# Kernel optimization log

Hardware: AMD Instinct MI355X
Metric: run time of the kernel (lower is better)

The kernel has to match this reference:

```python
import jax, jax.numpy as jnp
import numpy as np

DIM = 768
NUM_HEADS = 12
HEAD_DIM = DIM // NUM_HEADS
SCALE = HEAD_DIM ** -0.5
B, N = 8, 1024


def setup_inputs() -> dict:
    key = jax.random.key(0)
    k1, k2, k3, k4 = jax.random.split(key, 4)
    s = 1.0 / np.sqrt(DIM)
    return {
        "x": jax.random.normal(k1, (B, N, DIM), dtype=jnp.float32),
        "w_qkv": jax.random.normal(k2, (DIM, 3 * DIM), dtype=jnp.float32) * s,  # qkv_bias=False
        "w_proj": jax.random.normal(k3, (DIM, DIM), dtype=jnp.float32) * s,
        "b_proj": jax.random.normal(k4, (DIM,), dtype=jnp.float32) * 0.01,
    }


def reference(x, w_qkv, w_proj, b_proj):
    Bb, Nn, C = x.shape
    qkv = x @ w_qkv  # [B, N, 3C]
    qkv = qkv.reshape(Bb, Nn, 3, NUM_HEADS, HEAD_DIM)
    q = qkv[:, :, 0].transpose(0, 2, 1, 3)  # [B, H, N, d]
    k = qkv[:, :, 1].transpose(0, 2, 1, 3)
    v = qkv[:, :, 2].transpose(0, 2, 1, 3)
    attn = jnp.einsum("bhqd,bhkd->bhqk", q, k) * SCALE
    attn = jax.nn.softmax(attn, axis=-1)  # dropout p=0 -> identity
    out = jnp.einsum("bhqk,bhkd->bhqd", attn, v)
    out = out.transpose(0, 2, 1, 3).reshape(Bb, Nn, C)
    return out @ w_proj + b_proj
```

## Files before the change

### kernel.cpp

```cpp
#include <hip/hip_runtime.h>
#include <stdint.h>

typedef __attribute__((ext_vector_type(8))) __bf16 bf16x8;
typedef __attribute__((ext_vector_type(8))) unsigned short u16x8;
typedef __attribute__((ext_vector_type(4))) unsigned short u16x4;
typedef __attribute__((ext_vector_type(4))) short s16x4;
typedef __attribute__((ext_vector_type(4))) float f32x4;

typedef unsigned int u32_as1 __attribute__((address_space(1)));
typedef unsigned int u32_as3 __attribute__((address_space(3)));

__device__ __forceinline__ unsigned short f2bf(float f) {
  unsigned int u = __float_as_uint(f);
  u += 0x7fffu + ((u >> 16) & 1u);
  return (unsigned short)(u >> 16);
}

__device__ __forceinline__ bf16x8 ld_frag(const unsigned short* p) {
  return __builtin_bit_cast(bf16x8, *(const u16x8*)p);
}

__device__ __forceinline__ f32x4 mfma16(s16x4 a, s16x4 b, f32x4 c) {
#if __has_builtin(__builtin_amdgcn_mfma_f32_16x16x16bf16_1k)
  return __builtin_amdgcn_mfma_f32_16x16x16bf16_1k(a, b, c, 0, 0, 0);
#elif __has_builtin(__builtin_amdgcn_mfma_f32_16x16x16_bf16_1k)
  return __builtin_amdgcn_mfma_f32_16x16x16_bf16_1k(a, b, c, 0, 0, 0);
#else
  asm volatile("v_mfma_f32_16x16x16_bf16 %0, %1, %2, %0"
               : "+v"(c) : "v"(a), "v"(b));
  return c;
#endif
}

__device__ __forceinline__ float fast_exp2(float x) {
#if __has_builtin(__builtin_amdgcn_exp2f)
  return __builtin_amdgcn_exp2f(x);
#else
  return exp2f(x);
#endif
}

__device__ __forceinline__ void async16(const void* g, void* l) {
  const u32_as1* gp = (const u32_as1*)(uintptr_t)g;
  u32_as3* lp = (u32_as3*)(uintptr_t)l;
  __builtin_amdgcn_global_load_lds(gp, lp, 16, 0, 0);
}

__global__ __launch_bounds__(256) void prep_kernel(
    const float* __restrict__ x, const float* __restrict__ w_qkv,
    const float* __restrict__ w_proj, u16x4* __restrict__ x_bf,
    unsigned short* __restrict__ wqkvT, unsigned short* __restrict__ wprojT) {
  const int bid = blockIdx.x;
  const int t = threadIdx.x;
  if (bid < 6144) {
    const int i = bid * 256 + t;
    float4 v = ((const float4*)x)[i];
    u16x4 o;
    o[0] = f2bf(v.x); o[1] = f2bf(v.y); o[2] = f2bf(v.z); o[3] = f2bf(v.w);
    x_bf[i] = o;
    return;
  }
  __shared__ float tile[32][33];
  const float* w; unsigned short* wt; int N, bx, by;
  if (bid < 6144 + 1728) { const int r = bid - 6144; w = w_qkv; wt = wqkvT; N = 2304; bx = r % 72; by = r / 72; }
  else                   { const int r = bid - 7872; w = w_proj; wt = wprojT; N = 768; bx = r % 24; by = r / 24; }
  const int n0 = bx * 32, k0 = by * 32;
  const int tx = t & 31, ty = t >> 5;
#pragma unroll
  for (int r = 0; r < 4; r++)
    tile[ty + r * 8][tx] = w[(k0 + ty + r * 8) * N + n0 + tx];
  __syncthreads();
#pragma unroll
  for (int r = 0; r < 4; r++)
    wt[(n0 + ty + r * 8) * 768 + k0 + tx] = f2bf(tile[tx][ty + r * 8]);
}

template <int EPI, int NT, int NBLK>
__global__ __launch_bounds__(256, 4) void gemm_bt(
    const unsigned short* __restrict__ A, const unsigned short* __restrict__ Bt,
    unsigned short* __restrict__ qb, unsigned short* __restrict__ kb,
    unsigned short* __restrict__ vtb, float* __restrict__ outp,
    const float* __restrict__ bias) {
  __shared__ unsigned short As[128 * 32];
  __shared__ unsigned short Bs[NT * 64 * 32];
  const int t = threadIdx.x;
  const int lane = t & 63, w = t >> 6;
  const int quad = lane >> 4, l15 = lane & 15;

  const int bid = blockIdx.x;
  const int xcd = bid & 7, slot = bid >> 3;
  const int m0 = (xcd * 8 + slot / NBLK) * 128;
  const int n0 = (slot % NBLK) * (NT * 64);
  const int wm = (w & 1) * 64, wn = (w >> 1) * (NT * 32);

  f32x4 acc[4][NT * 2];
  const f32x4 fzero = {0.f, 0.f, 0.f, 0.f};
#pragma unroll
  for (int i = 0; i < 4; i++)
#pragma unroll
    for (int j = 0; j < NT * 2; j++) acc[i][j] = fzero;

  const int srow = w * 16 + (lane >> 2);
  const int scol = (((lane & 3) - (srow >> 1)) & 3) * 8;
  const unsigned short* Ag = A + (m0 + srow) * 768 + scol;
  const unsigned short* Bg = Bt + (n0 + srow) * 768 + scol;
  unsigned short* Asl = As + w * 512 + lane * 8;
  unsigned short* Bsl = Bs + w * 512 + lane * 8;

  for (int k0 = 0; k0 < 768; k0 += 32) {
    __syncthreads();
    async16(Ag + k0, Asl);
    async16(Ag + 64 * 768 + k0, Asl + 2048);
#pragma unroll
    for (int f = 0; f < NT; f++)
      async16(Bg + f * 64 * 768 + k0, Bsl + f * 2048);
    __syncthreads();

    bf16x8 af[4], bfr[NT * 2];
#pragma unroll
    for (int i = 0; i < 4; i++) {
      const int row = wm + i * 16 + l15;
      af[i] = ld_frag(As + row * 32 + (((quad + (row >> 1)) & 3) << 3));
    }
#pragma unroll
    for (int j = 0; j < NT * 2; j++) {
      const int row = wn + j * 16 + l15;
      bfr[j] = ld_frag(Bs + row * 32 + (((quad + (row >> 1)) & 3) << 3));
    }
#pragma unroll
    for (int i = 0; i < 4; i++)
#pragma unroll
      for (int j = 0; j < NT * 2; j++)
        acc[i][j] = __builtin_amdgcn_mfma_f32_16x16x32_bf16(af[i], bfr[j], acc[i][j], 0, 0, 0);
  }

#pragma unroll
  for (int i = 0; i < 4; i++) {
    const int gmb = m0 + wm + i * 16 + quad * 4;
#pragma unroll
    for (int j = 0; j < NT * 2; j++) {
      const int gc = n0 + wn + j * 16 + l15;
#pragma unroll
      for (int r = 0; r < 4; r++) {
        const int gm = gmb + r;
        float v = acc[i][j][r];
        if (EPI == 0) {
          const int b = gm >> 10, tok = gm & 1023;
          const int which = (gc >= 1536) ? 2 : (gc >= 768 ? 1 : 0);
          const int rem = gc - which * 768;
          const int h = rem >> 6, d = rem & 63;
          const int bh = b * 12 + h;
          const unsigned short bv = f2bf(v);
          if (which == 0)      qb[(bh << 16) + (tok << 6) + d] = bv;
          else if (which == 1) kb[(bh << 16) + (tok << 6) + d] = bv;
          else                 vtb[(bh << 16) + (d << 10) + tok] = bv;
        } else {
          outp[gm * 768 + gc] = v + bias[gc];
        }
      }
    }
  }
}

#define SWZC(row, c) (((row) << 6) + ((((c) + (row)) & 7) << 3))
#define C2 0.1803368801111244f

__global__ __launch_bounds__(256, 3) void attn_kernel(
    const unsigned short* __restrict__ qb, const unsigned short* __restrict__ kb,
    const unsigned short* __restrict__ vtb, unsigned short* __restrict__ aout) {
  __shared__ unsigned short smem[9216];
  unsigned short* Ks = smem;
  unsigned short* Vts = smem + 4096;

  const int t = threadIdx.x;
  const int lane = t & 63, w = t >> 6;
  const int quad = lane >> 4, l15 = lane & 15;
  const int bh = blockIdx.x;
  const int b = bh / 12, h = bh - b * 12;
  const int q0 = blockIdx.y * 128;
  const int base = bh << 16;

  bf16x8 qf[2][2];
#pragma unroll
  for (int qt = 0; qt < 2; qt++)
#pragma unroll
    for (int s = 0; s < 2; s++)
      qf[qt][s] = ld_frag(qb + base + ((q0 + w * 32 + qt * 16 + l15) << 6) +
                          s * 32 + quad * 8);

  f32x4 oacc[4][2];
  const f32x4 fzero = {0.f, 0.f, 0.f, 0.f};
#pragma unroll
  for (int dt = 0; dt < 4; dt++) { oacc[dt][0] = fzero; oacc[dt][1] = fzero; }
  float lsum0 = 0.f, lsum1 = 0.f;

  const int srow = t >> 3, schk = t & 7;
  const int c0 = ((schk - srow) & 7) * 8;
  const int c1 = ((schk - (srow + 32)) & 7) * 8;

  for (int kv0 = 0; kv0 < 1024; kv0 += 64) {
    __syncthreads();
    async16(kb + base + ((kv0 + srow) << 6) + c0, Ks + t * 8);
    async16(kb + base + ((kv0 + srow + 32) << 6) + c1, Ks + 2048 + t * 8);
    async16(vtb + base + (srow << 10) + kv0 + c0, Vts + t * 8);
    async16(vtb + base + ((srow + 32) << 10) + kv0 + c1, Vts + 2048 + t * 8);
    __syncthreads();

    f32x4 st[4][2];
#pragma unroll
    for (int tc = 0; tc < 4; tc++) { st[tc][0] = fzero; st[tc][1] = fzero; }
#pragma unroll
    for (int s = 0; s < 2; s++) {
#pragma unroll
      for (int tc = 0; tc < 4; tc++) {
        const bf16x8 kf = ld_frag(Ks + SWZC(tc * 16 + l15, s * 4 + quad));
        st[tc][0] = __builtin_amdgcn_mfma_f32_16x16x32_bf16(kf, qf[0][s], st[tc][0], 0, 0, 0);
        st[tc][1] = __builtin_amdgcn_mfma_f32_16x16x32_bf16(kf, qf[1][s], st[tc][1], 0, 0, 0);
      }
    }

    s16x4 pf[4][2];
#pragma unroll
    for (int tc = 0; tc < 4; tc++) {
#pragma unroll
      for (int qt = 0; qt < 2; qt++) {
        const float p0 = fast_exp2(st[tc][qt][0] * C2);
        const float p1 = fast_exp2(st[tc][qt][1] * C2);
        const float p2 = fast_exp2(st[tc][qt][2] * C2);
        const float p3 = fast_exp2(st[tc][qt][3] * C2);
        const float ps = (p0 + p1) + (p2 + p3);
        if (qt == 0) lsum0 += ps; else lsum1 += ps;
        s16x4 pk;
        pk[0] = (short)f2bf(p0); pk[1] = (short)f2bf(p1);
        pk[2] = (short)f2bf(p2); pk[3] = (short)f2bf(p3);
        pf[tc][qt] = pk;
      }
    }

#pragma unroll
    for (int tc = 0; tc < 4; tc++) {
#pragma unroll
      for (int dt = 0; dt < 4; dt++) {
        const int row = dt * 16 + l15;
        const int addr = (row << 6) + ((((tc * 2 + (quad >> 1)) + row) & 7) << 3) +
                         ((quad & 1) << 2);
        const s16x4 vf = *(const s16x4*)(Vts + addr);
        oacc[dt][0] = mfma16(vf, pf[tc][0], oacc[dt][0]);
        oacc[dt][1] = mfma16(vf, pf[tc][1], oacc[dt][1]);
      }
    }
  }

  lsum0 += __shfl_xor(lsum0, 16); lsum0 += __shfl_xor(lsum0, 32);
  lsum1 += __shfl_xor(lsum1, 16); lsum1 += __shfl_xor(lsum1, 32);
  const float inv0 = 1.f / lsum0, inv1 = 1.f / lsum1;

  __syncthreads();
  unsigned short* Ot = smem;
#pragma unroll
  for (int dt = 0; dt < 4; dt++) {
#pragma unroll
    for (int qt = 0; qt < 2; qt++) {
      const float inv = qt == 0 ? inv0 : inv1;
      const int qrow = (w * 32 + qt * 16 + l15) * 72 + dt * 16 + quad * 4;
#pragma unroll
      for (int r = 0; r < 4; r++)
        Ot[qrow + r] = f2bf(oacc[dt][qt][r] * inv);
    }
  }
  __syncthreads();
#pragma unroll
  for (int it = 0; it < 4; it++) {
    const int q = it * 32 + (t >> 3);
    const int d0 = (t & 7) * 8;
    const u16x8 v = *(const u16x8*)(Ot + q * 72 + d0);
    *(u16x8*)(aout + (b * 1024 + q0 + q) * 768 + h * 64 + d0) = v;
  }
}

extern "C" void kernel_launch(void* const* d_in, const int* in_sizes, int n_in,
                              void* d_out, int out_size, void* d_ws, size_t ws_size,
                              hipStream_t stream) {
  (void)in_sizes; (void)n_in; (void)out_size; (void)ws_size;
  const float* x = (const float*)d_in[0];
  const float* w_qkv = (const float*)d_in[1];
  const float* w_proj = (const float*)d_in[2];
  const float* b_proj = (const float*)d_in[3];
  float* out = (float*)d_out;

  char* ws = (char*)d_ws;
  unsigned short* x_bf   = (unsigned short*)(ws);
  unsigned short* wqkvT  = (unsigned short*)(ws + 12582912);
  unsigned short* wprojT = (unsigned short*)(ws + 16121856);
  unsigned short* qb     = (unsigned short*)(ws + 17301504);
  unsigned short* kb     = (unsigned short*)(ws + 29884416);
  unsigned short* vtb    = (unsigned short*)(ws + 42467328);
  unsigned short* aout   = x_bf;

  prep_kernel<<<8448, 256, 0, stream>>>(x, w_qkv, w_proj, (u16x4*)x_bf, wqkvT, wprojT);
  gemm_bt<0, 2, 18><<<1152, 256, 0, stream>>>(x_bf, wqkvT, qb, kb, vtb, nullptr, nullptr);
  attn_kernel<<<dim3(96, 8), 256, 0, stream>>>(qb, kb, vtb, aout);
  gemm_bt<1, 1, 12><<<768, 256, 0, stream>>>(aout, wprojT, nullptr, nullptr, nullptr, out, b_proj);
}
```

Baseline: 211.1 us.

## Triple-buffer LDS tiles with async prefetch in GEMM and attention kernels

Replaces the single-buffer load/sync/compute loops in the GEMM and attention kernels with a three-stage LDS ring. Tiles are prefetched two iterations ahead using global_load_lds, with an explicit vmcnt wait and a raw barrier per iteration. This lets memory latency overlap with MFMA work instead of stalling on two __syncthreads per tile. The cost is roughly three times the LDS footprint, which may lower occupancy (the attention kernel grows from about 18KB to 48KB). It also depends on the hand-counted vmcnt values being correct.

```diff
diff --git a/kernel.cpp b/kernel.cpp
--- a/kernel.cpp
+++ b/kernel.cpp
@@ -44,6 +44,15 @@
   const u32_as1* gp = (const u32_as1*)(uintptr_t)g;
   u32_as3* lp = (u32_as3*)(uintptr_t)l;
   __builtin_amdgcn_global_load_lds(gp, lp, 16, 0, 0);
+}
+
+template <int N> __device__ __forceinline__ void wait_vmcnt() {
+  if constexpr (N == 0) asm volatile("s_waitcnt vmcnt(0)" ::: "memory");
+  else if constexpr (N == 3) asm volatile("s_waitcnt vmcnt(3)" ::: "memory");
+  else if constexpr (N == 4) asm volatile("s_waitcnt vmcnt(4)" ::: "memory");
+}
+__device__ __forceinline__ void barrier_raw() {
+  asm volatile("s_barrier" ::: "memory");
 }
 
 __global__ __launch_bounds__(256) void prep_kernel(
@@ -81,8 +90,11 @@
     unsigned short* __restrict__ qb, unsigned short* __restrict__ kb,
     unsigned short* __restrict__ vtb, float* __restrict__ outp,
     const float* __restrict__ bias) {
-  __shared__ unsigned short As[128 * 32];
-  __shared__ unsigned short Bs[NT * 64 * 32];
+  constexpr int STAGE = 4096 + NT * 2048;
+  constexpr int NK = 24;
+  constexpr int NL = NT + 2;
+  __shared__ unsigned short smem[3 * STAGE];
+
   const int t = threadIdx.x;
   const int lane = t & 63, w = t >> 6;
   const int quad = lane >> 4, l15 = lane & 15;
@@ -104,17 +116,31 @@
   const int scol = (((lane & 3) - (srow >> 1)) & 3) * 8;
   const unsigned short* Ag = A + (m0 + srow) * 768 + scol;
   const unsigned short* Bg = Bt + (n0 + srow) * 768 + scol;
-  unsigned short* Asl = As + w * 512 + lane * 8;
-  unsigned short* Bsl = Bs + w * 512 + lane * 8;
-
-  for (int k0 = 0; k0 < 768; k0 += 32) {
-    __syncthreads();
-    async16(Ag + k0, Asl);
-    async16(Ag + 64 * 768 + k0, Asl + 2048);
+  const int ldso = w * 512 + lane * 8;
+
+  auto fill = [&](int ktile, int buf) {
+    const int kcol = ktile * 32;
+    unsigned short* As = smem + buf * STAGE;
+    unsigned short* Bs = As + 4096;
+    async16(Ag + kcol, As + ldso);
+    async16(Ag + 64 * 768 + kcol, As + ldso + 2048);
 #pragma unroll
     for (int f = 0; f < NT; f++)
-      async16(Bg + f * 64 * 768 + k0, Bsl + f * 2048);
-    __syncthreads();
+      async16(Bg + f * 64 * 768 + kcol, Bs + ldso + f * 2048);
+  };
+
+  fill(0, 0);
+  fill(1, 1);
+  int cur = 0;
+  for (int k = 0; k < NK; ++k) {
+    if (k < NK - 1) wait_vmcnt<NL>(); else wait_vmcnt<0>();
+    barrier_raw();
+    if (k + 2 < NK) {
+      int tgt = cur + 2; if (tgt >= 3) tgt -= 3;
+      fill(k + 2, tgt);
+    }
+    const unsigned short* As = smem + cur * STAGE;
+    const unsigned short* Bs = As + 4096;
 
     bf16x8 af[4], bfr[NT * 2];
 #pragma unroll
@@ -132,6 +158,8 @@
 #pragma unroll
       for (int j = 0; j < NT * 2; j++)
         acc[i][j] = __builtin_amdgcn_mfma_f32_16x16x32_bf16(af[i], bfr[j], acc[i][j], 0, 0, 0);
+
+    cur += 1; if (cur == 3) cur = 0;
   }
 
 #pragma unroll
@@ -168,9 +196,7 @@
 __global__ __launch_bounds__(256, 3) void attn_kernel(
     const unsigned short* __restrict__ qb, const unsigned short* __restrict__ kb,
     const unsigned short* __restrict__ vtb, unsigned short* __restrict__ aout) {
-  __shared__ unsigned short smem[9216];
-  unsigned short* Ks = smem;
-  unsigned short* Vts = smem + 4096;
+  __shared__ unsigned short smem[3 * 8192];
 
   const int t = threadIdx.x;
   const int lane = t & 63, w = t >> 6;
@@ -198,13 +224,28 @@
   const int c0 = ((schk - srow) & 7) * 8;
   const int c1 = ((schk - (srow + 32)) & 7) * 8;
 
-  for (int kv0 = 0; kv0 < 1024; kv0 += 64) {
-    __syncthreads();
+  auto fillkv = [&](int tile, int buf) {
+    const int kv0 = tile * 64;
+    unsigned short* Ks = smem + buf * 8192;
+    unsigned short* Vts = Ks + 4096;
     async16(kb + base + ((kv0 + srow) << 6) + c0, Ks + t * 8);
     async16(kb + base + ((kv0 + srow + 32) << 6) + c1, Ks + 2048 + t * 8);
     async16(vtb + base + (srow << 10) + kv0 + c0, Vts + t * 8);
     async16(vtb + base + ((srow + 32) << 10) + kv0 + c1, Vts + 2048 + t * 8);
-    __syncthreads();
+  };
+
+  fillkv(0, 0);
+  fillkv(1, 1);
+  int cur = 0;
+  for (int it = 0; it < 16; ++it) {
+    if (it < 15) wait_vmcnt<4>(); else wait_vmcnt<0>();
+    barrier_raw();
+    if (it + 2 < 16) {
+      int tgt = cur + 2; if (tgt >= 3) tgt -= 3;
+      fillkv(it + 2, tgt);
+    }
+    const unsigned short* Ks = smem + cur * 8192;
+    const unsigned short* Vts = Ks + 4096;
 
     f32x4 st[4][2];
 #pragma unroll
@@ -249,6 +290,8 @@
         oacc[dt][1] = mfma16(vf, pf[tc][1], oacc[dt][1]);
       }
     }
+
+    cur += 1; if (cur == 3) cur = 0;
   }
 
   lsum0 += __shfl_xor(lsum0, 16); lsum0 += __shfl_xor(lsum0, 32);
```

After: 202.4 us. 1.04x faster.
